# Performance work log

Hardware: AMD Instinct MI355X
Metric: run time of the kernel (lower is better)

Reference implementation:

```python
import jax, jax.numpy as jnp
import numpy as np

# physical and transform constants (from BVPModel fields / zpinn globals)
_C0 = 343.0   # speed of sound
_RHO0 = 1.21  # air density (unused in r_net)
FC, F0 = 500.0, 100.0
XC, YC, ZC = 0.7, 0.5, 0.6
AC, A0 = 2.0, 0.1
BC, B0 = 1.5, -0.05

N = 131072
H = 256


def setup_inputs() -> dict:
    key = jax.random.key(0)
    ks = jax.random.split(key, 10)
    inp = {
        "x": jax.random.uniform(ks[0], (N,), jnp.float32),
        "y": jax.random.uniform(ks[1], (N,), jnp.float32),
        "z": jax.random.uniform(ks[2], (N,), jnp.float32),
        "f": jax.random.uniform(ks[3], (N,), jnp.float32),
        # MLP params, scaled by 1/sqrt(fan_in) (glorot-ish)
        "W1": jax.random.normal(ks[4], (H, 4), jnp.float32) / np.sqrt(4.0),
        "b1": jnp.zeros((H,), jnp.float32),
        "W2": jax.random.normal(ks[5], (H, H), jnp.float32) / np.sqrt(H),
        "b2": jnp.zeros((H,), jnp.float32),
        "W3": jax.random.normal(ks[6], (H, H), jnp.float32) / np.sqrt(H),
        "b3": jnp.zeros((H,), jnp.float32),
        "W4": jax.random.normal(ks[7], (2, H), jnp.float32) / np.sqrt(H),
        "b4": jnp.zeros((2,), jnp.float32),
    }
    return inp


def _psi(params, x, y, z, f):
    """Scalar-coordinate MLP: psi(x,y,z,f) -> (2,) [real, imag]."""
    h = jnp.stack([x, y, z, f])
    for (W, b) in params[:-1]:
        h = jnp.tanh(W @ h + b)
    W, b = params[-1]
    return W @ h + b


def reference(x, y, z, f, W1, b1, W2, b2, W3, b3, W4, b4):
    params = ((W1, b1), (W2, b2), (W3, b3), (W4, b4))

    def r_net(xi, yi, zi, fi):
        k = 2.0 * jnp.pi * (fi * FC + F0) / _C0
        pr, pi = _psi(params, xi, yi, zi, fi)

        fr = lambda a, b_, c, d: _psi(params, a, b_, c, d)[0]
        fim = lambda a, b_, c, d: _psi(params, a, b_, c, d)[1]
        d2 = lambda fn, i: jax.grad(jax.grad(fn, i), i)

        p_xxr = d2(fr, 0)(xi, yi, zi, fi)
        p_yyr = d2(fr, 1)(xi, yi, zi, fi)
        p_zzr = d2(fr, 2)(xi, yi, zi, fi)
        res_re = AC * ((YC * ZC) ** 2 * p_xxr
                       + (XC * ZC) ** 2 * p_yyr
                       + (XC * YC) ** 2 * p_zzr) \
            + (XC * YC * ZC * k) ** 2 * (pr * AC + A0)

        p_xxi = d2(fim, 0)(xi, yi, zi, fi)
        p_yyi = d2(fim, 1)(xi, yi, zi, fi)
        p_zzi = d2(fim, 2)(xi, yi, zi, fi)
        res_im = BC * ((YC * ZC) ** 2 * p_xxi
                       + (XC * ZC) ** 2 * p_yyi
                       + (XC * YC) ** 2 * p_zzi) \
            + (XC * YC * ZC * k) ** 2 * (pi * BC + B0)
        return res_re, res_im

    rr, ri = jax.vmap(r_net)(x, y, z, f)
    return jnp.stack([rr, ri])  # (2, N)
```

## Files before the change

kernel.cpp:

```cpp
#include <hip/hip_runtime.h>
#include <math.h>


typedef __attribute__((ext_vector_type(8))) short short8;
typedef __attribute__((ext_vector_type(4))) float floatx4;
typedef unsigned short ushort_t;
typedef unsigned int uint_t;

#define PBLK 16

__device__ __forceinline__ ushort_t f2bf(float f) {
    uint_t u = __float_as_uint(f);
    return (ushort_t)((u + 0x7FFFu + ((u >> 16) & 1u)) >> 16);
}
__device__ __forceinline__ uint_t pack2bf(float f0, float f1) {
    uint_t u0 = __float_as_uint(f0) + 0x8000u;
    uint_t u1 = __float_as_uint(f1) + 0x8000u;
    return __builtin_amdgcn_perm(u1, u0, 0x07060302u);
}
__device__ __forceinline__ float fast_tanh(float u) {
    float e = __expf(2.f * u);
    return 1.f - 2.f / (e + 1.f);
}

__global__ void prep_split(const float* __restrict__ W2, const float* __restrict__ W3,
                           short8* __restrict__ ws) {
    int t16 = blockIdx.x * blockDim.x + threadIdx.x;
    int lane = t16 & 63;
    int kc = (t16 >> 6) & 7;
    int tt = (t16 >> 9) & 15;
    int l = t16 >> 13;
    const float* W = l ? W3 : W2;
    int row = tt * 16 + (lane & 15);
    int qa = lane >> 4;
    const float* src = W + row * 256 + kc * 32 + (l ? 4 * qa : 8 * qa);
    float4 va = *(const float4*)src;
    float4 vb = *(const float4*)(src + (l ? 16 : 4));
    float v[8] = {va.x, va.y, va.z, va.w, vb.x, vb.y, vb.z, vb.w};
    short8 hi8;
    #pragma unroll
    for (int j = 0; j < 8; ++j) hi8[j] = (short)f2bf(v[j]);
    ws[l * 8192 + tt * 512 + kc * 64 + lane] = hi8;
}

__global__ __launch_bounds__(512, 4)
void bvp_main(const float* __restrict__ gx, const float* __restrict__ gy,
              const float* __restrict__ gz, const float* __restrict__ gf,
              const float* __restrict__ W1, const float* __restrict__ b1,
              const float* __restrict__ b2, const float* __restrict__ b3,
              const float* __restrict__ W4, const float* __restrict__ b4,
              const short8* __restrict__ wsA, float* __restrict__ out, int N) {
    __shared__ short8 Bsh[7 * 8 * 64];
    __shared__ float red[8][16][8];

    const int tid = threadIdx.x;
    const int w = tid >> 6, lane = tid & 63;
    const int n15 = lane & 15, qc = lane >> 4;
    const int pbase = blockIdx.x * PBLK;
    const short8* __restrict__ wsA3 = wsA + 8192;

    floatx4 acc[2][7];
    short8 a0[2], a1[2];

    #pragma unroll
    for (int rt = 0; rt < 2; ++rt) a0[rt] = wsA[(2 * w + rt) * 512 + lane];

    {
        const int pp = tid & 15, u8 = tid >> 4;
        const int pidx = min(pbase + pp, N - 1);
        const float xi = gx[pidx], yi = gy[pidx], zi = gz[pidx], fi = gf[pidx];
        float hv[7][8];
        #pragma unroll
        for (int r = 0; r < 8; ++r) {
            const int i = u8 * 8 + r;
            float4 wv = *(const float4*)(W1 + 4 * i);
            float u = fmaf(wv.x, xi, fmaf(wv.y, yi, fmaf(wv.z, zi, fmaf(wv.w, fi, b1[i]))));
            float t = fast_tanh(u), s = 1.f - t * t, c = -2.f * t * s;
            hv[0][r] = t;
            hv[1][r] = s * wv.x; hv[2][r] = s * wv.y; hv[3][r] = s * wv.z;
            hv[4][r] = c * wv.x * wv.x; hv[5][r] = c * wv.y * wv.y; hv[6][r] = c * wv.z * wv.z;
        }
        const int kt = u8 >> 2, qb = u8 & 3;
        #pragma unroll
        for (int s = 0; s < 7; ++s) {
            union { short8 s8; uint_t u4[4]; } v;
            #pragma unroll
            for (int j = 0; j < 4; ++j)
                v.u4[j] = pack2bf(hv[s][2 * j], hv[s][2 * j + 1]);
            Bsh[(s * 8 + kt) * 64 + qb * 16 + pp] = v.s8;
        }
    }
    __syncthreads();

    auto run_gemm = [&](const short8* __restrict__ A) {
        #pragma unroll
        for (int rt = 0; rt < 2; ++rt)
            #pragma unroll
            for (int ct = 0; ct < 7; ++ct) acc[rt][ct] = (floatx4){0.f, 0.f, 0.f, 0.f};
        #pragma unroll
        for (int kc = 0; kc < 8; ++kc) {
            if (kc < 7) {
                #pragma unroll
                for (int rt = 0; rt < 2; ++rt)
                    a1[rt] = A[(2 * w + rt) * 512 + (kc + 1) * 64 + lane];
            }
            short8 b[7];
            #pragma unroll
            for (int ct = 0; ct < 7; ++ct) b[ct] = Bsh[(ct * 8 + kc) * 64 + lane];
            #pragma unroll
            for (int ct = 0; ct < 7; ++ct)
                #pragma unroll
                for (int rt = 0; rt < 2; ++rt)
                    acc[rt][ct] = __builtin_amdgcn_mfma_f32_16x16x32_bf16(a0[rt], b[ct], acc[rt][ct], 0, 0, 0);
            if (kc < 7) {
                #pragma unroll
                for (int rt = 0; rt < 2; ++rt) a0[rt] = a1[rt];
            }
        }
    };

    run_gemm(wsA);
    __syncthreads();

    #pragma unroll
    for (int rt = 0; rt < 2; ++rt) a0[rt] = wsA3[(2 * w + rt) * 512 + lane];

    #pragma unroll
    for (int rt = 0; rt < 2; ++rt) {
        const float4 bb = *(const float4*)(b2 + w * 32 + rt * 16 + qc * 4);
        const float bbv[4] = {bb.x, bb.y, bb.z, bb.w};
        #pragma unroll
        for (int r = 0; r < 4; ++r) {
            float t = fast_tanh(acc[rt][0][r] + bbv[r]);
            float s = 1.f - t * t, c = -2.f * t * s;
            float ux = acc[rt][1][r], uy = acc[rt][2][r], uz = acc[rt][3][r];
            acc[rt][0][r] = t;
            acc[rt][1][r] = s * ux; acc[rt][2][r] = s * uy; acc[rt][3][r] = s * uz;
            acc[rt][4][r] = fmaf(s, acc[rt][4][r], c * ux * ux);
            acc[rt][5][r] = fmaf(s, acc[rt][5][r], c * uy * uy);
            acc[rt][6][r] = fmaf(s, acc[rt][6][r], c * uz * uz);
        }
    }
    #pragma unroll
    for (int s = 0; s < 7; ++s) {
        union { short8 s8; uint_t u4[4]; } v;
        v.u4[0] = pack2bf(acc[0][s][0], acc[0][s][1]);
        v.u4[1] = pack2bf(acc[0][s][2], acc[0][s][3]);
        v.u4[2] = pack2bf(acc[1][s][0], acc[1][s][1]);
        v.u4[3] = pack2bf(acc[1][s][2], acc[1][s][3]);
        Bsh[(s * 8 + w) * 64 + lane] = v.s8;
    }
    __syncthreads();

    run_gemm(wsA3);

    float pt[8] = {0.f, 0.f, 0.f, 0.f, 0.f, 0.f, 0.f, 0.f};
    #pragma unroll
    for (int rt = 0; rt < 2; ++rt) {
        const int rb = w * 32 + rt * 16 + qc * 4;
        const float4 bb = *(const float4*)(b3 + rb);
        const float4 w0 = *(const float4*)(W4 + rb);
        const float4 w1 = *(const float4*)(W4 + 256 + rb);
        const float bbv[4] = {bb.x, bb.y, bb.z, bb.w};
        const float w0v[4] = {w0.x, w0.y, w0.z, w0.w};
        const float w1v[4] = {w1.x, w1.y, w1.z, w1.w};
        #pragma unroll
        for (int r = 0; r < 4; ++r) {
            float t = fast_tanh(acc[rt][0][r] + bbv[r]);
            float s = 1.f - t * t, c = -2.f * t * s;
            float ux = acc[rt][1][r], uy = acc[rt][2][r], uz = acc[rt][3][r];
            float hv = t;
            float hxx = fmaf(s, acc[rt][4][r], c * ux * ux);
            float hyy = fmaf(s, acc[rt][5][r], c * uy * uy);
            float hzz = fmaf(s, acc[rt][6][r], c * uz * uz);
            pt[0] = fmaf(w0v[r], hv, pt[0]);
            pt[1] = fmaf(w0v[r], hxx, pt[1]);
            pt[2] = fmaf(w0v[r], hyy, pt[2]);
            pt[3] = fmaf(w0v[r], hzz, pt[3]);
            pt[4] = fmaf(w1v[r], hv, pt[4]);
            pt[5] = fmaf(w1v[r], hxx, pt[5]);
            pt[6] = fmaf(w1v[r], hyy, pt[6]);
            pt[7] = fmaf(w1v[r], hzz, pt[7]);
        }
    }
    #pragma unroll
    for (int k = 0; k < 8; ++k) {
        pt[k] += __shfl_xor(pt[k], 16, 64);
        pt[k] += __shfl_xor(pt[k], 32, 64);
    }
    if (qc == 0) {
        *(float4*)&red[w][n15][0] = make_float4(pt[0], pt[1], pt[2], pt[3]);
        *(float4*)&red[w][n15][4] = make_float4(pt[4], pt[5], pt[6], pt[7]);
    }
    __syncthreads();

    if (tid < 16 && (pbase + tid) < N) {
        const int n = pbase + tid;
        float s8[8] = {0.f, 0.f, 0.f, 0.f, 0.f, 0.f, 0.f, 0.f};
        #pragma unroll
        for (int ww = 0; ww < 8; ++ww)
            #pragma unroll
            for (int k = 0; k < 8; ++k) s8[k] += red[ww][tid][k];
        const float fi = gf[n];
        const float PI = 3.14159265358979323846f;
        const float kw = 2.f * PI * (fi * 500.f + 100.f) / 343.f;
        const float vol = 0.7f * 0.5f * 0.6f;
        const float kk = vol * vol * kw * kw;
        const float cxx = (0.5f * 0.6f) * (0.5f * 0.6f);
        const float cyy = (0.7f * 0.6f) * (0.7f * 0.6f);
        const float czz = (0.7f * 0.5f) * (0.7f * 0.5f);
        const float pr = s8[0] + b4[0];
        const float pim = s8[4] + b4[1];
        out[n]     = 2.0f * (cxx * s8[1] + cyy * s8[2] + czz * s8[3]) + kk * (pr * 2.0f + 0.1f);
        out[N + n] = 1.5f * (cxx * s8[5] + cyy * s8[6] + czz * s8[7]) + kk * (pim * 1.5f - 0.05f);
    }
}

extern "C" void kernel_launch(void* const* d_in, const int* in_sizes, int n_in,
                              void* d_out, int out_size, void* d_ws, size_t ws_size,
                              hipStream_t stream) {
    const float* x = (const float*)d_in[0];
    const float* y = (const float*)d_in[1];
    const float* z = (const float*)d_in[2];
    const float* f = (const float*)d_in[3];
    const float* W1 = (const float*)d_in[4];
    const float* b1 = (const float*)d_in[5];
    const float* W2 = (const float*)d_in[6];
    const float* b2 = (const float*)d_in[7];
    const float* W3 = (const float*)d_in[8];
    const float* b3 = (const float*)d_in[9];
    const float* W4 = (const float*)d_in[10];
    const float* b4 = (const float*)d_in[11];
    float* out = (float*)d_out;
    const int N = in_sizes[0];
    const int grid = (N + PBLK - 1) / PBLK;

    prep_split<<<64, 256, 0, stream>>>(W2, W3, (short8*)d_ws);
    bvp_main<<<grid, 512, 0, stream>>>(x, y, z, f, W1, b1, b2, b3, W4, b4,
                                       (const short8*)d_ws, out, N);
}
```

Before: 320.0 us.

## Run two point-groups per block in skewed stages to overlap GEMM and elementwise phases

```diff
diff --git a/kernel.cpp b/kernel.cpp
--- a/kernel.cpp
+++ b/kernel.cpp
@@ -7,7 +7,7 @@
 typedef unsigned short ushort_t;
 typedef unsigned int uint_t;
 
-#define PBLK 16
+#define PBLK 32
 
 __device__ __forceinline__ ushort_t f2bf(float f) {
     uint_t u = __float_as_uint(f);
@@ -43,30 +43,60 @@
     ws[l * 8192 + tt * 512 + kc * 64 + lane] = hi8;
 }
 
-__global__ __launch_bounds__(512, 4)
+__global__ __launch_bounds__(1024, 4)
 void bvp_main(const float* __restrict__ gx, const float* __restrict__ gy,
               const float* __restrict__ gz, const float* __restrict__ gf,
               const float* __restrict__ W1, const float* __restrict__ b1,
               const float* __restrict__ b2, const float* __restrict__ b3,
               const float* __restrict__ W4, const float* __restrict__ b4,
               const short8* __restrict__ wsA, float* __restrict__ out, int N) {
-    __shared__ short8 Bsh[7 * 8 * 64];
-    __shared__ float red[8][16][8];
+    __shared__ short8 Bsh[2][7 * 8 * 64];
+    __shared__ float red[2][8][16][8];
 
     const int tid = threadIdx.x;
     const int w = tid >> 6, lane = tid & 63;
+    const int grp = w >> 3;
+    const int wl = w & 7;
+    const int gt = tid & 511;
     const int n15 = lane & 15, qc = lane >> 4;
-    const int pbase = blockIdx.x * PBLK;
-    const short8* __restrict__ wsA3 = wsA + 8192;
+    const int pbase = blockIdx.x * PBLK + grp * 16;
+    short8* const __restrict__ Bg = Bsh[grp];
+    const short8* const __restrict__ wsA3 = wsA + 8192;
 
     floatx4 acc[2][7];
     short8 a0[2], a1[2];
 
-    #pragma unroll
-    for (int rt = 0; rt < 2; ++rt) a0[rt] = wsA[(2 * w + rt) * 512 + lane];
-
-    {
-        const int pp = tid & 15, u8 = tid >> 4;
+    auto run_gemm = [&](const short8* __restrict__ A) {
+        #pragma unroll
+        for (int rt = 0; rt < 2; ++rt)
+            #pragma unroll
+            for (int ct = 0; ct < 7; ++ct) acc[rt][ct] = (floatx4){0.f, 0.f, 0.f, 0.f};
+        #pragma unroll
+        for (int kc = 0; kc < 8; ++kc) {
+            if (kc < 7) {
+                #pragma unroll
+                for (int rt = 0; rt < 2; ++rt)
+                    a1[rt] = A[(2 * wl + rt) * 512 + (kc + 1) * 64 + lane];
+            }
+            short8 b[7];
+            #pragma unroll
+            for (int ct = 0; ct < 7; ++ct) b[ct] = Bg[(ct * 8 + kc) * 64 + lane];
+            #pragma unroll
+            for (int ct = 0; ct < 7; ++ct)
+                #pragma unroll
+                for (int rt = 0; rt < 2; ++rt)
+                    acc[rt][ct] = __builtin_amdgcn_mfma_f32_16x16x32_bf16(a0[rt], b[ct], acc[rt][ct], 0, 0, 0);
+            if (kc < 7) {
+                #pragma unroll
+                for (int rt = 0; rt < 2; ++rt) a0[rt] = a1[rt];
+            }
+        }
+    };
+
+    auto stage_l1 = [&]() {
+        #pragma unroll
+        for (int rt = 0; rt < 2; ++rt) a0[rt] = wsA[(2 * wl + rt) * 512 + lane];
+        const int pp = gt & 15, u8 = gt >> 4;
         const int pidx = min(pbase + pp, N - 1);
         const float xi = gx[pidx], yi = gy[pidx], zi = gz[pidx], fi = gf[pidx];
         float hv[7][8];
@@ -87,120 +117,99 @@
             #pragma unroll
             for (int j = 0; j < 4; ++j)
                 v.u4[j] = pack2bf(hv[s][2 * j], hv[s][2 * j + 1]);
-            Bsh[(s * 8 + kt) * 64 + qb * 16 + pp] = v.s8;
-        }
+            Bg[(s * 8 + kt) * 64 + qb * 16 + pp] = v.s8;
+        }
+    };
+
+    auto stage_j2 = [&]() {
+        #pragma unroll
+        for (int rt = 0; rt < 2; ++rt) a0[rt] = wsA3[(2 * wl + rt) * 512 + lane];
+        #pragma unroll
+        for (int rt = 0; rt < 2; ++rt) {
+            const float4 bb = *(const float4*)(b2 + wl * 32 + rt * 16 + qc * 4);
+            const float bbv[4] = {bb.x, bb.y, bb.z, bb.w};
+            #pragma unroll
+            for (int r = 0; r < 4; ++r) {
+                float t = fast_tanh(acc[rt][0][r] + bbv[r]);
+                float s = 1.f - t * t, c = -2.f * t * s;
+                float ux = acc[rt][1][r], uy = acc[rt][2][r], uz = acc[rt][3][r];
+                acc[rt][0][r] = t;
+                acc[rt][1][r] = s * ux; acc[rt][2][r] = s * uy; acc[rt][3][r] = s * uz;
+                acc[rt][4][r] = fmaf(s, acc[rt][4][r], c * ux * ux);
+                acc[rt][5][r] = fmaf(s, acc[rt][5][r], c * uy * uy);
+                acc[rt][6][r] = fmaf(s, acc[rt][6][r], c * uz * uz);
+            }
+        }
+        #pragma unroll
+        for (int s = 0; s < 7; ++s) {
+            union { short8 s8; uint_t u4[4]; } v;
+            v.u4[0] = pack2bf(acc[0][s][0], acc[0][s][1]);
+            v.u4[1] = pack2bf(acc[0][s][2], acc[0][s][3]);
+            v.u4[2] = pack2bf(acc[1][s][0], acc[1][s][1]);
+            v.u4[3] = pack2bf(acc[1][s][2], acc[1][s][3]);
+            Bg[(s * 8 + wl) * 64 + lane] = v.s8;
+        }
+    };
+
+    auto stage_j3 = [&]() {
+        float pt[8] = {0.f, 0.f, 0.f, 0.f, 0.f, 0.f, 0.f, 0.f};
+        #pragma unroll
+        for (int rt = 0; rt < 2; ++rt) {
+            const int rb = wl * 32 + rt * 16 + qc * 4;
+            const float4 bb = *(const float4*)(b3 + rb);
+            const float4 w0 = *(const float4*)(W4 + rb);
+            const float4 w1 = *(const float4*)(W4 + 256 + rb);
+            const float bbv[4] = {bb.x, bb.y, bb.z, bb.w};
+            const float w0v[4] = {w0.x, w0.y, w0.z, w0.w};
+            const float w1v[4] = {w1.x, w1.y, w1.z, w1.w};
+            #pragma unroll
+            for (int r = 0; r < 4; ++r) {
+                float t = fast_tanh(acc[rt][0][r] + bbv[r]);
+                float s = 1.f - t * t, c = -2.f * t * s;
+                float ux = acc[rt][1][r], uy = acc[rt][2][r], uz = acc[rt][3][r];
+                float hvv = t;
+                float hxx = fmaf(s, acc[rt][4][r], c * ux * ux);
+                float hyy = fmaf(s, acc[rt][5][r], c * uy * uy);
+                float hzz = fmaf(s, acc[rt][6][r], c * uz * uz);
+                pt[0] = fmaf(w0v[r], hvv, pt[0]);
+                pt[1] = fmaf(w0v[r], hxx, pt[1]);
+                pt[2] = fmaf(w0v[r], hyy, pt[2]);
+                pt[3] = fmaf(w0v[r], hzz, pt[3]);
+                pt[4] = fmaf(w1v[r], hvv, pt[4]);
+                pt[5] = fmaf(w1v[r], hxx, pt[5]);
+                pt[6] = fmaf(w1v[r], hyy, pt[6]);
+                pt[7] = fmaf(w1v[r], hzz, pt[7]);
+            }
+        }
+        #pragma unroll
+        for (int k = 0; k < 8; ++k) {
+            pt[k] += __shfl_xor(pt[k], 16, 64);
+            pt[k] += __shfl_xor(pt[k], 32, 64);
+        }
+        if (qc == 0) {
+            *(float4*)&red[grp][wl][n15][0] = make_float4(pt[0], pt[1], pt[2], pt[3]);
+            *(float4*)&red[grp][wl][n15][4] = make_float4(pt[4], pt[5], pt[6], pt[7]);
+        }
+    };
+
+    #pragma unroll 1
+    for (int ph = 0; ph < 6; ++ph) {
+        const int st = ph - grp;
+        if (st == 0)      stage_l1();
+        else if (st == 1) run_gemm(wsA);
+        else if (st == 2) stage_j2();
+        else if (st == 3) run_gemm(wsA3);
+        else if (st == 4) stage_j3();
+        __syncthreads();
     }
-    __syncthreads();
-
-    auto run_gemm = [&](const short8* __restrict__ A) {
-        #pragma unroll
-        for (int rt = 0; rt < 2; ++rt)
-            #pragma unroll
-            for (int ct = 0; ct < 7; ++ct) acc[rt][ct] = (floatx4){0.f, 0.f, 0.f, 0.f};
-        #pragma unroll
-        for (int kc = 0; kc < 8; ++kc) {
-            if (kc < 7) {
-                #pragma unroll
-                for (int rt = 0; rt < 2; ++rt)
-                    a1[rt] = A[(2 * w + rt) * 512 + (kc + 1) * 64 + lane];
-            }
-            short8 b[7];
-            #pragma unroll
-            for (int ct = 0; ct < 7; ++ct) b[ct] = Bsh[(ct * 8 + kc) * 64 + lane];
-            #pragma unroll
-            for (int ct = 0; ct < 7; ++ct)
-                #pragma unroll
-                for (int rt = 0; rt < 2; ++rt)
-                    acc[rt][ct] = __builtin_amdgcn_mfma_f32_16x16x32_bf16(a0[rt], b[ct], acc[rt][ct], 0, 0, 0);
-            if (kc < 7) {
-                #pragma unroll
-                for (int rt = 0; rt < 2; ++rt) a0[rt] = a1[rt];
-            }
-        }
-    };
-
-    run_gemm(wsA);
-    __syncthreads();
-
-    #pragma unroll
-    for (int rt = 0; rt < 2; ++rt) a0[rt] = wsA3[(2 * w + rt) * 512 + lane];
-
-    #pragma unroll
-    for (int rt = 0; rt < 2; ++rt) {
-        const float4 bb = *(const float4*)(b2 + w * 32 + rt * 16 + qc * 4);
-        const float bbv[4] = {bb.x, bb.y, bb.z, bb.w};
-        #pragma unroll
-        for (int r = 0; r < 4; ++r) {
-            float t = fast_tanh(acc[rt][0][r] + bbv[r]);
-            float s = 1.f - t * t, c = -2.f * t * s;
-            float ux = acc[rt][1][r], uy = acc[rt][2][r], uz = acc[rt][3][r];
-            acc[rt][0][r] = t;
-            acc[rt][1][r] = s * ux; acc[rt][2][r] = s * uy; acc[rt][3][r] = s * uz;
-            acc[rt][4][r] = fmaf(s, acc[rt][4][r], c * ux * ux);
-            acc[rt][5][r] = fmaf(s, acc[rt][5][r], c * uy * uy);
-            acc[rt][6][r] = fmaf(s, acc[rt][6][r], c * uz * uz);
-        }
-    }
-    #pragma unroll
-    for (int s = 0; s < 7; ++s) {
-        union { short8 s8; uint_t u4[4]; } v;
-        v.u4[0] = pack2bf(acc[0][s][0], acc[0][s][1]);
-        v.u4[1] = pack2bf(acc[0][s][2], acc[0][s][3]);
-        v.u4[2] = pack2bf(acc[1][s][0], acc[1][s][1]);
-        v.u4[3] = pack2bf(acc[1][s][2], acc[1][s][3]);
-        Bsh[(s * 8 + w) * 64 + lane] = v.s8;
-    }
-    __syncthreads();
-
-    run_gemm(wsA3);
-
-    float pt[8] = {0.f, 0.f, 0.f, 0.f, 0.f, 0.f, 0.f, 0.f};
-    #pragma unroll
-    for (int rt = 0; rt < 2; ++rt) {
-        const int rb = w * 32 + rt * 16 + qc * 4;
-        const float4 bb = *(const float4*)(b3 + rb);
-        const float4 w0 = *(const float4*)(W4 + rb);
-        const float4 w1 = *(const float4*)(W4 + 256 + rb);
-        const float bbv[4] = {bb.x, bb.y, bb.z, bb.w};
-        const float w0v[4] = {w0.x, w0.y, w0.z, w0.w};
-        const float w1v[4] = {w1.x, w1.y, w1.z, w1.w};
-        #pragma unroll
-        for (int r = 0; r < 4; ++r) {
-            float t = fast_tanh(acc[rt][0][r] + bbv[r]);
-            float s = 1.f - t * t, c = -2.f * t * s;
-            float ux = acc[rt][1][r], uy = acc[rt][2][r], uz = acc[rt][3][r];
-            float hv = t;
-            float hxx = fmaf(s, acc[rt][4][r], c * ux * ux);
-            float hyy = fmaf(s, acc[rt][5][r], c * uy * uy);
-            float hzz = fmaf(s, acc[rt][6][r], c * uz * uz);
-            pt[0] = fmaf(w0v[r], hv, pt[0]);
-            pt[1] = fmaf(w0v[r], hxx, pt[1]);
-            pt[2] = fmaf(w0v[r], hyy, pt[2]);
-            pt[3] = fmaf(w0v[r], hzz, pt[3]);
-            pt[4] = fmaf(w1v[r], hv, pt[4]);
-            pt[5] = fmaf(w1v[r], hxx, pt[5]);
-            pt[6] = fmaf(w1v[r], hyy, pt[6]);
-            pt[7] = fmaf(w1v[r], hzz, pt[7]);
-        }
-    }
-    #pragma unroll
-    for (int k = 0; k < 8; ++k) {
-        pt[k] += __shfl_xor(pt[k], 16, 64);
-        pt[k] += __shfl_xor(pt[k], 32, 64);
-    }
-    if (qc == 0) {
-        *(float4*)&red[w][n15][0] = make_float4(pt[0], pt[1], pt[2], pt[3]);
-        *(float4*)&red[w][n15][4] = make_float4(pt[4], pt[5], pt[6], pt[7]);
-    }
-    __syncthreads();
-
-    if (tid < 16 && (pbase + tid) < N) {
-        const int n = pbase + tid;
+
+    if (gt < 16 && (pbase + gt) < N) {
+        const int n = pbase + gt;
         float s8[8] = {0.f, 0.f, 0.f, 0.f, 0.f, 0.f, 0.f, 0.f};
         #pragma unroll
         for (int ww = 0; ww < 8; ++ww)
             #pragma unroll
-            for (int k = 0; k < 8; ++k) s8[k] += red[ww][tid][k];
+            for (int k = 0; k < 8; ++k) s8[k] += red[grp][ww][gt][k];
         const float fi = gf[n];
         const float PI = 3.14159265358979323846f;
         const float kw = 2.f * PI * (fi * 500.f + 100.f) / 343.f;
@@ -236,6 +245,6 @@
     const int grid = (N + PBLK - 1) / PBLK;
 
     prep_split<<<64, 256, 0, stream>>>(W2, W3, (short8*)d_ws);
-    bvp_main<<<grid, 512, 0, stream>>>(x, y, z, f, W1, b1, b2, b3, W4, b4,
-                                       (const short8*)d_ws, out, N);
-}
+    bvp_main<<<grid, 1024, 0, stream>>>(x, y, z, f, W1, b1, b2, b3, W4, b4,
+                                        (const short8*)d_ws, out, N);
+}
```

Result: slower. 806.3 us (+152.0%).

## Make blocks persistent over 8 point groups with a software-pipelined layer-2/3 GEMM

Applied to the files above, without the earlier changes.

```diff
diff --git a/kernel.cpp b/kernel.cpp
--- a/kernel.cpp
+++ b/kernel.cpp
@@ -7,7 +7,8 @@
 typedef unsigned short ushort_t;
 typedef unsigned int uint_t;
 
-#define PBLK 16
+#define GPB 8
+#define PBLK (16 * GPB)
 
 __device__ __forceinline__ ushort_t f2bf(float f) {
     uint_t u = __float_as_uint(f);
@@ -43,36 +44,33 @@
     ws[l * 8192 + tt * 512 + kc * 64 + lane] = hi8;
 }
 
-__global__ __launch_bounds__(512, 4)
+__global__ __launch_bounds__(512, 1)
 void bvp_main(const float* __restrict__ gx, const float* __restrict__ gy,
               const float* __restrict__ gz, const float* __restrict__ gf,
               const float* __restrict__ W1, const float* __restrict__ b1,
               const float* __restrict__ b2, const float* __restrict__ b3,
               const float* __restrict__ W4, const float* __restrict__ b4,
               const short8* __restrict__ wsA, float* __restrict__ out, int N) {
-    __shared__ short8 Bsh[7 * 8 * 64];
+    __shared__ short8 B1sh[7 * 8 * 64];
+    __shared__ short8 B2sh[7 * 8 * 64];
     __shared__ float red[8][16][8];
 
     const int tid = threadIdx.x;
     const int w = tid >> 6, lane = tid & 63;
     const int n15 = lane & 15, qc = lane >> 4;
-    const int pbase = blockIdx.x * PBLK;
+    const int blockbase = blockIdx.x * PBLK;
     const short8* __restrict__ wsA3 = wsA + 8192;
 
-    floatx4 acc[2][7];
-    short8 a0[2], a1[2];
-
-    #pragma unroll
-    for (int rt = 0; rt < 2; ++rt) a0[rt] = wsA[(2 * w + rt) * 512 + lane];
-
-    {
-        const int pp = tid & 15, u8 = tid >> 4;
-        const int pidx = min(pbase + pp, N - 1);
-        const float xi = gx[pidx], yi = gy[pidx], zi = gz[pidx], fi = gf[pidx];
+    floatx4 acc2[2][7];
+    floatx4 acc3[2][7];
+    short8 a2c[2], a3c[2];
+
+    auto stage_l1 = [&](float xi, float yi, float zi, float fi) {
+        const int pp = tid & 15, u8g = tid >> 4;
         float hv[7][8];
         #pragma unroll
         for (int r = 0; r < 8; ++r) {
-            const int i = u8 * 8 + r;
+            const int i = u8g * 8 + r;
             float4 wv = *(const float4*)(W1 + 4 * i);
             float u = fmaf(wv.x, xi, fmaf(wv.y, yi, fmaf(wv.z, zi, fmaf(wv.w, fi, b1[i]))));
             float t = fast_tanh(u), s = 1.f - t * t, c = -2.f * t * s;
@@ -80,23 +78,31 @@
             hv[1][r] = s * wv.x; hv[2][r] = s * wv.y; hv[3][r] = s * wv.z;
             hv[4][r] = c * wv.x * wv.x; hv[5][r] = c * wv.y * wv.y; hv[6][r] = c * wv.z * wv.z;
         }
-        const int kt = u8 >> 2, qb = u8 & 3;
+        const int kt = u8g >> 2, qb = u8g & 3;
         #pragma unroll
         for (int s = 0; s < 7; ++s) {
             union { short8 s8; uint_t u4[4]; } v;
             #pragma unroll
             for (int j = 0; j < 4; ++j)
                 v.u4[j] = pack2bf(hv[s][2 * j], hv[s][2 * j + 1]);
-            Bsh[(s * 8 + kt) * 64 + qb * 16 + pp] = v.s8;
-        }
-    }
-    __syncthreads();
-
-    auto run_gemm = [&](const short8* __restrict__ A) {
+            B1sh[(s * 8 + kt) * 64 + qb * 16 + pp] = v.s8;
+        }
+    };
+
+    auto load_a0 = [&]() {
+        #pragma unroll
+        for (int rt = 0; rt < 2; ++rt) a2c[rt] = wsA[(2 * w + rt) * 512 + lane];
+        #pragma unroll
+        for (int rt = 0; rt < 2; ++rt) a3c[rt] = wsA3[(2 * w + rt) * 512 + lane];
+    };
+
+    auto gemm_one = [&](const short8* __restrict__ A, const short8* __restrict__ Bs,
+                        floatx4 (&acc)[2][7], short8 (&ac)[2]) {
         #pragma unroll
         for (int rt = 0; rt < 2; ++rt)
             #pragma unroll
             for (int ct = 0; ct < 7; ++ct) acc[rt][ct] = (floatx4){0.f, 0.f, 0.f, 0.f};
+        short8 a0[2] = {ac[0], ac[1]}, a1[2];
         #pragma unroll
         for (int kc = 0; kc < 8; ++kc) {
             if (kc < 7) {
@@ -106,7 +112,7 @@
             }
             short8 b[7];
             #pragma unroll
-            for (int ct = 0; ct < 7; ++ct) b[ct] = Bsh[(ct * 8 + kc) * 64 + lane];
+            for (int ct = 0; ct < 7; ++ct) b[ct] = Bs[(ct * 8 + kc) * 64 + lane];
             #pragma unroll
             for (int ct = 0; ct < 7; ++ct)
                 #pragma unroll
@@ -119,101 +125,179 @@
         }
     };
 
-    run_gemm(wsA);
-    __syncthreads();
-
-    #pragma unroll
-    for (int rt = 0; rt < 2; ++rt) a0[rt] = wsA3[(2 * w + rt) * 512 + lane];
-
-    #pragma unroll
-    for (int rt = 0; rt < 2; ++rt) {
-        const float4 bb = *(const float4*)(b2 + w * 32 + rt * 16 + qc * 4);
-        const float bbv[4] = {bb.x, bb.y, bb.z, bb.w};
-        #pragma unroll
-        for (int r = 0; r < 4; ++r) {
-            float t = fast_tanh(acc[rt][0][r] + bbv[r]);
-            float s = 1.f - t * t, c = -2.f * t * s;
-            float ux = acc[rt][1][r], uy = acc[rt][2][r], uz = acc[rt][3][r];
-            acc[rt][0][r] = t;
-            acc[rt][1][r] = s * ux; acc[rt][2][r] = s * uy; acc[rt][3][r] = s * uz;
-            acc[rt][4][r] = fmaf(s, acc[rt][4][r], c * ux * ux);
-            acc[rt][5][r] = fmaf(s, acc[rt][5][r], c * uy * uy);
-            acc[rt][6][r] = fmaf(s, acc[rt][6][r], c * uz * uz);
-        }
-    }
-    #pragma unroll
-    for (int s = 0; s < 7; ++s) {
-        union { short8 s8; uint_t u4[4]; } v;
-        v.u4[0] = pack2bf(acc[0][s][0], acc[0][s][1]);
-        v.u4[1] = pack2bf(acc[0][s][2], acc[0][s][3]);
-        v.u4[2] = pack2bf(acc[1][s][0], acc[1][s][1]);
-        v.u4[3] = pack2bf(acc[1][s][2], acc[1][s][3]);
-        Bsh[(s * 8 + w) * 64 + lane] = v.s8;
+    auto gemm_fused = [&]() {
+        #pragma unroll
+        for (int rt = 0; rt < 2; ++rt)
+            #pragma unroll
+            for (int ct = 0; ct < 7; ++ct) {
+                acc2[rt][ct] = (floatx4){0.f, 0.f, 0.f, 0.f};
+                acc3[rt][ct] = (floatx4){0.f, 0.f, 0.f, 0.f};
+            }
+        short8 a20[2] = {a2c[0], a2c[1]}, a30[2] = {a3c[0], a3c[1]};
+        short8 a21[2], a31[2];
+        #pragma unroll
+        for (int kc = 0; kc < 8; ++kc) {
+            if (kc < 7) {
+                #pragma unroll
+                for (int rt = 0; rt < 2; ++rt) {
+                    a21[rt] = wsA[(2 * w + rt) * 512 + (kc + 1) * 64 + lane];
+                    a31[rt] = wsA3[(2 * w + rt) * 512 + (kc + 1) * 64 + lane];
+                }
+            }
+            short8 b1f[7];
+            #pragma unroll
+            for (int ct = 0; ct < 7; ++ct) b1f[ct] = B1sh[(ct * 8 + kc) * 64 + lane];
+            #pragma unroll
+            for (int ct = 0; ct < 7; ++ct)
+                #pragma unroll
+                for (int rt = 0; rt < 2; ++rt)
+                    acc2[rt][ct] = __builtin_amdgcn_mfma_f32_16x16x32_bf16(a20[rt], b1f[ct], acc2[rt][ct], 0, 0, 0);
+            short8 b2f[7];
+            #pragma unroll
+            for (int ct = 0; ct < 7; ++ct) b2f[ct] = B2sh[(ct * 8 + kc) * 64 + lane];
+            #pragma unroll
+            for (int ct = 0; ct < 7; ++ct)
+                #pragma unroll
+                for (int rt = 0; rt < 2; ++rt)
+                    acc3[rt][ct] = __builtin_amdgcn_mfma_f32_16x16x32_bf16(a30[rt], b2f[ct], acc3[rt][ct], 0, 0, 0);
+            if (kc < 7) {
+                #pragma unroll
+                for (int rt = 0; rt < 2; ++rt) { a20[rt] = a21[rt]; a30[rt] = a31[rt]; }
+            }
+        }
+    };
+
+    auto jet2 = [&]() {
+        #pragma unroll
+        for (int rt = 0; rt < 2; ++rt) {
+            const float4 bb = *(const float4*)(b2 + w * 32 + rt * 16 + qc * 4);
+            const float bbv[4] = {bb.x, bb.y, bb.z, bb.w};
+            #pragma unroll
+            for (int r = 0; r < 4; ++r) {
+                float t = fast_tanh(acc2[rt][0][r] + bbv[r]);
+                float s = 1.f - t * t, c = -2.f * t * s;
+                float ux = acc2[rt][1][r], uy = acc2[rt][2][r], uz = acc2[rt][3][r];
+                acc2[rt][0][r] = t;
+                acc2[rt][1][r] = s * ux; acc2[rt][2][r] = s * uy; acc2[rt][3][r] = s * uz;
+                acc2[rt][4][r] = fmaf(s, acc2[rt][4][r], c * ux * ux);
+                acc2[rt][5][r] = fmaf(s, acc2[rt][5][r], c * uy * uy);
+                acc2[rt][6][r] = fmaf(s, acc2[rt][6][r], c * uz * uz);
+            }
+        }
+        #pragma unroll
+        for (int s = 0; s < 7; ++s) {
+            union { short8 s8; uint_t u4[4]; } v;
+            v.u4[0] = pack2bf(acc2[0][s][0], acc2[0][s][1]);
+            v.u4[1] = pack2bf(acc2[0][s][2], acc2[0][s][3]);
+            v.u4[2] = pack2bf(acc2[1][s][0], acc2[1][s][1]);
+            v.u4[3] = pack2bf(acc2[1][s][2], acc2[1][s][3]);
+            B2sh[(s * 8 + w) * 64 + lane] = v.s8;
+        }
+    };
+
+    auto jet3red = [&]() {
+        float pt[8] = {0.f, 0.f, 0.f, 0.f, 0.f, 0.f, 0.f, 0.f};
+        #pragma unroll
+        for (int rt = 0; rt < 2; ++rt) {
+            const int rb = w * 32 + rt * 16 + qc * 4;
+            const float4 bb = *(const float4*)(b3 + rb);
+            const float4 w0 = *(const float4*)(W4 + rb);
+            const float4 w1 = *(const float4*)(W4 + 256 + rb);
+            const float bbv[4] = {bb.x, bb.y, bb.z, bb.w};
+            const float w0v[4] = {w0.x, w0.y, w0.z, w0.w};
+            const float w1v[4] = {w1.x, w1.y, w1.z, w1.w};
+            #pragma unroll
+            for (int r = 0; r < 4; ++r) {
+                float t = fast_tanh(acc3[rt][0][r] + bbv[r]);
+                float s = 1.f - t * t, c = -2.f * t * s;
+                float ux = acc3[rt][1][r], uy = acc3[rt][2][r], uz = acc3[rt][3][r];
+                float hv = t;
+                float hxx = fmaf(s, acc3[rt][4][r], c * ux * ux);
+                float hyy = fmaf(s, acc3[rt][5][r], c * uy * uy);
+                float hzz = fmaf(s, acc3[rt][6][r], c * uz * uz);
+                pt[0] = fmaf(w0v[r], hv, pt[0]);
+                pt[1] = fmaf(w0v[r], hxx, pt[1]);
+                pt[2] = fmaf(w0v[r], hyy, pt[2]);
+                pt[3] = fmaf(w0v[r], hzz, pt[3]);
+                pt[4] = fmaf(w1v[r], hv, pt[4]);
+                pt[5] = fmaf(w1v[r], hxx, pt[5]);
+                pt[6] = fmaf(w1v[r], hyy, pt[6]);
+                pt[7] = fmaf(w1v[r], hzz, pt[7]);
+            }
+        }
+        #pragma unroll
+        for (int k = 0; k < 8; ++k) {
+            pt[k] += __shfl_xor(pt[k], 16, 64);
+            pt[k] += __shfl_xor(pt[k], 32, 64);
+        }
+        if (qc == 0) {
+            *(float4*)&red[w][n15][0] = make_float4(pt[0], pt[1], pt[2], pt[3]);
+            *(float4*)&red[w][n15][4] = make_float4(pt[4], pt[5], pt[6], pt[7]);
+        }
+    };
+
+    auto finalout = [&](int gb) {
+        if (tid < 16 && (gb + tid) < N) {
+            const int n = gb + tid;
+            float s8[8] = {0.f, 0.f, 0.f, 0.f, 0.f, 0.f, 0.f, 0.f};
+            #pragma unroll
+            for (int ww = 0; ww < 8; ++ww)
+                #pragma unroll
+                for (int k = 0; k < 8; ++k) s8[k] += red[ww][tid][k];
+            const float fi = gf[n];
+            const float PI = 3.14159265358979323846f;
+            const float kw = 2.f * PI * (fi * 500.f + 100.f) / 343.f;
+            const float vol = 0.7f * 0.5f * 0.6f;
+            const float kk = vol * vol * kw * kw;
+            const float cxx = (0.5f * 0.6f) * (0.5f * 0.6f);
+            const float cyy = (0.7f * 0.6f) * (0.7f * 0.6f);
+            const float czz = (0.7f * 0.5f) * (0.7f * 0.5f);
+            const float pr = s8[0] + b4[0];
+            const float pim = s8[4] + b4[1];
+            out[n]     = 2.0f * (cxx * s8[1] + cyy * s8[2] + czz * s8[3]) + kk * (pr * 2.0f + 0.1f);
+            out[N + n] = 1.5f * (cxx * s8[5] + cyy * s8[6] + czz * s8[7]) + kk * (pim * 1.5f - 0.05f);
+        }
+    };
+
+    {
+        const int p0 = min(blockbase + (tid & 15), N - 1);
+        #pragma unroll
+        for (int rt = 0; rt < 2; ++rt) a2c[rt] = wsA[(2 * w + rt) * 512 + lane];
+        stage_l1(gx[p0], gy[p0], gz[p0], gf[p0]);
     }
     __syncthreads();
 
-    run_gemm(wsA3);
-
-    float pt[8] = {0.f, 0.f, 0.f, 0.f, 0.f, 0.f, 0.f, 0.f};
-    #pragma unroll
-    for (int rt = 0; rt < 2; ++rt) {
-        const int rb = w * 32 + rt * 16 + qc * 4;
-        const float4 bb = *(const float4*)(b3 + rb);
-        const float4 w0 = *(const float4*)(W4 + rb);
-        const float4 w1 = *(const float4*)(W4 + 256 + rb);
-        const float bbv[4] = {bb.x, bb.y, bb.z, bb.w};
-        const float w0v[4] = {w0.x, w0.y, w0.z, w0.w};
-        const float w1v[4] = {w1.x, w1.y, w1.z, w1.w};
-        #pragma unroll
-        for (int r = 0; r < 4; ++r) {
-            float t = fast_tanh(acc[rt][0][r] + bbv[r]);
-            float s = 1.f - t * t, c = -2.f * t * s;
-            float ux = acc[rt][1][r], uy = acc[rt][2][r], uz = acc[rt][3][r];
-            float hv = t;
-            float hxx = fmaf(s, acc[rt][4][r], c * ux * ux);
-            float hyy = fmaf(s, acc[rt][5][r], c * uy * uy);
-            float hzz = fmaf(s, acc[rt][6][r], c * uz * uz);
-            pt[0] = fmaf(w0v[r], hv, pt[0]);
-            pt[1] = fmaf(w0v[r], hxx, pt[1]);
-            pt[2] = fmaf(w0v[r], hyy, pt[2]);
-            pt[3] = fmaf(w0v[r], hzz, pt[3]);
-            pt[4] = fmaf(w1v[r], hv, pt[4]);
-            pt[5] = fmaf(w1v[r], hxx, pt[5]);
-            pt[6] = fmaf(w1v[r], hyy, pt[6]);
-            pt[7] = fmaf(w1v[r], hzz, pt[7]);
-        }
+    {
+        const int p1i = min(blockbase + 16 + (tid & 15), N - 1);
+        const float x1 = gx[p1i], y1 = gy[p1i], z1 = gz[p1i], f1 = gf[p1i];
+        gemm_one(wsA, B1sh, acc2, a2c);
+        __syncthreads();
+        load_a0();
+        jet2();
+        __syncthreads();
+        stage_l1(x1, y1, z1, f1);
+        __syncthreads();
     }
-    #pragma unroll
-    for (int k = 0; k < 8; ++k) {
-        pt[k] += __shfl_xor(pt[k], 16, 64);
-        pt[k] += __shfl_xor(pt[k], 32, 64);
+
+    #pragma unroll 1
+    for (int i = 1; i < GPB; ++i) {
+        const int pn = min(blockbase + (i + 1) * 16 + (tid & 15), N - 1);
+        const float xn = gx[pn], yn = gy[pn], zn = gz[pn], fn = gf[pn];
+        gemm_fused();
+        __syncthreads();
+        load_a0();
+        jet2();
+        jet3red();
+        __syncthreads();
+        finalout(blockbase + (i - 1) * 16);
+        if (i < GPB - 1) stage_l1(xn, yn, zn, fn);
+        __syncthreads();
     }
-    if (qc == 0) {
-        *(float4*)&red[w][n15][0] = make_float4(pt[0], pt[1], pt[2], pt[3]);
-        *(float4*)&red[w][n15][4] = make_float4(pt[4], pt[5], pt[6], pt[7]);
-    }
+
+    gemm_one(wsA3, B2sh, acc3, a3c);
+    jet3red();
     __syncthreads();
-
-    if (tid < 16 && (pbase + tid) < N) {
-        const int n = pbase + tid;
-        float s8[8] = {0.f, 0.f, 0.f, 0.f, 0.f, 0.f, 0.f, 0.f};
-        #pragma unroll
-        for (int ww = 0; ww < 8; ++ww)
-            #pragma unroll
-            for (int k = 0; k < 8; ++k) s8[k] += red[ww][tid][k];
-        const float fi = gf[n];
-        const float PI = 3.14159265358979323846f;
-        const float kw = 2.f * PI * (fi * 500.f + 100.f) / 343.f;
-        const float vol = 0.7f * 0.5f * 0.6f;
-        const float kk = vol * vol * kw * kw;
-        const float cxx = (0.5f * 0.6f) * (0.5f * 0.6f);
-        const float cyy = (0.7f * 0.6f) * (0.7f * 0.6f);
-        const float czz = (0.7f * 0.5f) * (0.7f * 0.5f);
-        const float pr = s8[0] + b4[0];
-        const float pim = s8[4] + b4[1];
-        out[n]     = 2.0f * (cxx * s8[1] + cyy * s8[2] + czz * s8[3]) + kk * (pr * 2.0f + 0.1f);
-        out[N + n] = 1.5f * (cxx * s8[5] + cyy * s8[6] + czz * s8[7]) + kk * (pim * 1.5f - 0.05f);
-    }
+    finalout(blockbase + (GPB - 1) * 16);
 }
 
 extern "C" void kernel_launch(void* const* d_in, const int* in_sizes, int n_in,
```

After: 653.8 us. 104% more time.

## Propagate weighted Laplacian instead of three separate second derivatives

Applied to the files above, without the earlier changes.

```diff
diff --git a/kernel.cpp b/kernel.cpp
--- a/kernel.cpp
+++ b/kernel.cpp
@@ -8,6 +8,11 @@
 typedef unsigned int uint_t;
 
 #define PBLK 16
+#define NS 5
+
+#define CXX 0.09f
+#define CYY 0.1764f
+#define CZZ 0.1225f
 
 __device__ __forceinline__ ushort_t f2bf(float f) {
     uint_t u = __float_as_uint(f);
@@ -50,8 +55,8 @@
               const float* __restrict__ b2, const float* __restrict__ b3,
               const float* __restrict__ W4, const float* __restrict__ b4,
               const short8* __restrict__ wsA, float* __restrict__ out, int N) {
-    __shared__ short8 Bsh[7 * 8 * 64];
-    __shared__ float red[8][16][8];
+    __shared__ short8 Bsh[NS * 8 * 64];
+    __shared__ float red[8][16][4];
 
     const int tid = threadIdx.x;
     const int w = tid >> 6, lane = tid & 63;
@@ -59,7 +64,7 @@
     const int pbase = blockIdx.x * PBLK;
     const short8* __restrict__ wsA3 = wsA + 8192;
 
-    floatx4 acc[2][7];
+    floatx4 acc[2][NS];
     short8 a0[2], a1[2];
 
     #pragma unroll
@@ -69,20 +74,21 @@
         const int pp = tid & 15, u8 = tid >> 4;
         const int pidx = min(pbase + pp, N - 1);
         const float xi = gx[pidx], yi = gy[pidx], zi = gz[pidx], fi = gf[pidx];
-        float hv[7][8];
+        float hv[NS][8];
         #pragma unroll
         for (int r = 0; r < 8; ++r) {
             const int i = u8 * 8 + r;
             float4 wv = *(const float4*)(W1 + 4 * i);
             float u = fmaf(wv.x, xi, fmaf(wv.y, yi, fmaf(wv.z, zi, fmaf(wv.w, fi, b1[i]))));
             float t = fast_tanh(u), s = 1.f - t * t, c = -2.f * t * s;
+            float wq = fmaf(CXX * wv.x, wv.x, fmaf(CYY * wv.y, wv.y, CZZ * wv.z * wv.z));
             hv[0][r] = t;
             hv[1][r] = s * wv.x; hv[2][r] = s * wv.y; hv[3][r] = s * wv.z;
-            hv[4][r] = c * wv.x * wv.x; hv[5][r] = c * wv.y * wv.y; hv[6][r] = c * wv.z * wv.z;
+            hv[4][r] = c * wq;
         }
         const int kt = u8 >> 2, qb = u8 & 3;
         #pragma unroll
-        for (int s = 0; s < 7; ++s) {
+        for (int s = 0; s < NS; ++s) {
             union { short8 s8; uint_t u4[4]; } v;
             #pragma unroll
             for (int j = 0; j < 4; ++j)
@@ -96,7 +102,7 @@
         #pragma unroll
         for (int rt = 0; rt < 2; ++rt)
             #pragma unroll
-            for (int ct = 0; ct < 7; ++ct) acc[rt][ct] = (floatx4){0.f, 0.f, 0.f, 0.f};
+            for (int ct = 0; ct < NS; ++ct) acc[rt][ct] = (floatx4){0.f, 0.f, 0.f, 0.f};
         #pragma unroll
         for (int kc = 0; kc < 8; ++kc) {
             if (kc < 7) {
@@ -104,11 +110,11 @@
                 for (int rt = 0; rt < 2; ++rt)
                     a1[rt] = A[(2 * w + rt) * 512 + (kc + 1) * 64 + lane];
             }
-            short8 b[7];
-            #pragma unroll
-            for (int ct = 0; ct < 7; ++ct) b[ct] = Bsh[(ct * 8 + kc) * 64 + lane];
-            #pragma unroll
-            for (int ct = 0; ct < 7; ++ct)
+            short8 b[NS];
+            #pragma unroll
+            for (int ct = 0; ct < NS; ++ct) b[ct] = Bsh[(ct * 8 + kc) * 64 + lane];
+            #pragma unroll
+            for (int ct = 0; ct < NS; ++ct)
                 #pragma unroll
                 for (int rt = 0; rt < 2; ++rt)
                     acc[rt][ct] = __builtin_amdgcn_mfma_f32_16x16x32_bf16(a0[rt], b[ct], acc[rt][ct], 0, 0, 0);
@@ -134,15 +140,14 @@
             float t = fast_tanh(acc[rt][0][r] + bbv[r]);
             float s = 1.f - t * t, c = -2.f * t * s;
             float ux = acc[rt][1][r], uy = acc[rt][2][r], uz = acc[rt][3][r];
+            float wq = fmaf(CXX * ux, ux, fmaf(CYY * uy, uy, CZZ * uz * uz));
             acc[rt][0][r] = t;
             acc[rt][1][r] = s * ux; acc[rt][2][r] = s * uy; acc[rt][3][r] = s * uz;
-            acc[rt][4][r] = fmaf(s, acc[rt][4][r], c * ux * ux);
-            acc[rt][5][r] = fmaf(s, acc[rt][5][r], c * uy * uy);
-            acc[rt][6][r] = fmaf(s, acc[rt][6][r], c * uz * uz);
-        }
-    }
-    #pragma unroll
-    for (int s = 0; s < 7; ++s) {
+            acc[rt][4][r] = fmaf(s, acc[rt][4][r], c * wq);
+        }
+    }
+    #pragma unroll
+    for (int s = 0; s < NS; ++s) {
         union { short8 s8; uint_t u4[4]; } v;
         v.u4[0] = pack2bf(acc[0][s][0], acc[0][s][1]);
         v.u4[1] = pack2bf(acc[0][s][2], acc[0][s][3]);
@@ -154,7 +159,7 @@
 
     run_gemm(wsA3);
 
-    float pt[8] = {0.f, 0.f, 0.f, 0.f, 0.f, 0.f, 0.f, 0.f};
+    float pt[4] = {0.f, 0.f, 0.f, 0.f};
     #pragma unroll
     for (int rt = 0; rt < 2; ++rt) {
         const int rb = w * 32 + rt * 16 + qc * 4;
@@ -169,50 +174,39 @@
             float t = fast_tanh(acc[rt][0][r] + bbv[r]);
             float s = 1.f - t * t, c = -2.f * t * s;
             float ux = acc[rt][1][r], uy = acc[rt][2][r], uz = acc[rt][3][r];
-            float hv = t;
-            float hxx = fmaf(s, acc[rt][4][r], c * ux * ux);
-            float hyy = fmaf(s, acc[rt][5][r], c * uy * uy);
-            float hzz = fmaf(s, acc[rt][6][r], c * uz * uz);
-            pt[0] = fmaf(w0v[r], hv, pt[0]);
-            pt[1] = fmaf(w0v[r], hxx, pt[1]);
-            pt[2] = fmaf(w0v[r], hyy, pt[2]);
-            pt[3] = fmaf(w0v[r], hzz, pt[3]);
-            pt[4] = fmaf(w1v[r], hv, pt[4]);
-            pt[5] = fmaf(w1v[r], hxx, pt[5]);
-            pt[6] = fmaf(w1v[r], hyy, pt[6]);
-            pt[7] = fmaf(w1v[r], hzz, pt[7]);
-        }
-    }
-    #pragma unroll
-    for (int k = 0; k < 8; ++k) {
+            float wq = fmaf(CXX * ux, ux, fmaf(CYY * uy, uy, CZZ * uz * uz));
+            float hL = fmaf(s, acc[rt][4][r], c * wq);
+            pt[0] = fmaf(w0v[r], t, pt[0]);
+            pt[1] = fmaf(w0v[r], hL, pt[1]);
+            pt[2] = fmaf(w1v[r], t, pt[2]);
+            pt[3] = fmaf(w1v[r], hL, pt[3]);
+        }
+    }
+    #pragma unroll
+    for (int k = 0; k < 4; ++k) {
         pt[k] += __shfl_xor(pt[k], 16, 64);
         pt[k] += __shfl_xor(pt[k], 32, 64);
     }
-    if (qc == 0) {
+    if (qc == 0)
         *(float4*)&red[w][n15][0] = make_float4(pt[0], pt[1], pt[2], pt[3]);
-        *(float4*)&red[w][n15][4] = make_float4(pt[4], pt[5], pt[6], pt[7]);
-    }
     __syncthreads();
 
     if (tid < 16 && (pbase + tid) < N) {
         const int n = pbase + tid;
-        float s8[8] = {0.f, 0.f, 0.f, 0.f, 0.f, 0.f, 0.f, 0.f};
+        float s4[4] = {0.f, 0.f, 0.f, 0.f};
         #pragma unroll
         for (int ww = 0; ww < 8; ++ww)
             #pragma unroll
-            for (int k = 0; k < 8; ++k) s8[k] += red[ww][tid][k];
+            for (int k = 0; k < 4; ++k) s4[k] += red[ww][tid][k];
         const float fi = gf[n];
         const float PI = 3.14159265358979323846f;
         const float kw = 2.f * PI * (fi * 500.f + 100.f) / 343.f;
         const float vol = 0.7f * 0.5f * 0.6f;
         const float kk = vol * vol * kw * kw;
-        const float cxx = (0.5f * 0.6f) * (0.5f * 0.6f);
-        const float cyy = (0.7f * 0.6f) * (0.7f * 0.6f);
-        const float czz = (0.7f * 0.5f) * (0.7f * 0.5f);
-        const float pr = s8[0] + b4[0];
-        const float pim = s8[4] + b4[1];
-        out[n]     = 2.0f * (cxx * s8[1] + cyy * s8[2] + czz * s8[3]) + kk * (pr * 2.0f + 0.1f);
-        out[N + n] = 1.5f * (cxx * s8[5] + cyy * s8[6] + czz * s8[7]) + kk * (pim * 1.5f - 0.05f);
+        const float pr = s4[0] + b4[0];
+        const float pim = s4[2] + b4[1];
+        out[n]     = 2.0f * s4[1] + kk * (pr * 2.0f + 0.1f);
+        out[N + n] = 1.5f * s4[3] + kk * (pim * 1.5f - 0.05f);
     }
 }
 
```

New measurement: 265.4 us. 1.21x faster.
